# Optimization experiments

Measured on AMD Instinct MI355X. Metric: run time of the kernel, lower is better.

The kernel has to match this reference:

```python
import jax, jax.numpy as jnp
import numpy as np

ISO = 0.0
# cube corner k has coords ((k>>0)&1, (k>>1)&1, (k>>2)&1)
CORNERS = np.array([[(k >> 0) & 1, (k >> 1) & 1, (k >> 2) & 1] for k in range(8)], np.int32)
# 6-tetrahedra decomposition of the cube around body diagonal 0-7
TETS = np.array([[0,1,3,7],[0,3,2,7],[0,2,6,7],[0,6,4,7],[0,4,5,7],[0,5,1,7]], np.int32)
TET_EDGES = np.array([[0,1],[0,2],[0,3],[1,2],[1,3],[2,3]], np.int32)
# marching-tetrahedra triangle table: sign case -> up to 2 triangles of tet-edge ids (-1 = pad)
MT_TRI = np.array([
 [-1,-1,-1,-1,-1,-1],
 [0,1,2,-1,-1,-1],
 [0,3,4,-1,-1,-1],
 [1,2,4,1,4,3],
 [1,3,5,-1,-1,-1],
 [0,2,5,0,5,3],
 [0,1,5,0,5,4],
 [2,4,5,-1,-1,-1],
 [2,4,5,-1,-1,-1],
 [0,1,5,0,5,4],
 [0,3,5,0,5,2],
 [1,3,5,-1,-1,-1],
 [1,3,4,1,4,2],
 [0,3,4,-1,-1,-1],
 [0,1,2,-1,-1,-1],
 [-1,-1,-1,-1,-1,-1]], np.int32)

# map (tet, tet-edge) -> unique per-cell edge slot; enumerate unique corner pairs
_pairs, _edges = {}, []
T2C = np.zeros((6, 6), np.int32)
for _ti in range(6):
    for _ei in range(6):
        _a = int(TETS[_ti, TET_EDGES[_ei, 0]]); _b = int(TETS[_ti, TET_EDGES[_ei, 1]])
        _key = (min(_a, _b), max(_a, _b))
        if _key not in _pairs:
            _pairs[_key] = len(_edges); _edges.append(_key)
        T2C[_ti, _ei] = _pairs[_key]
CELL_EDGES = np.array(_edges, np.int32)  # (19, 2)
N_EDGE = len(_edges)


def _forward(sdfsgrid, featgrid, isovalue=ISO):
    X, Y, Z = sdfsgrid.shape
    F = featgrid.shape[-1]
    dt = sdfsgrid.dtype
    # pad like the torch wrapper: sdf border = isovalue+1 (outside), features = 0
    s = jnp.pad(sdfsgrid, 1, constant_values=isovalue + 1.0)
    f = jnp.pad(featgrid, ((1, 1), (1, 1), (1, 1), (0, 0)))
    cx, cy, cz = s.shape[0] - 1, s.shape[1] - 1, s.shape[2] - 1
    # per-cell corner values: (cx,cy,cz,8) and (cx,cy,cz,8,F)
    cs = jnp.stack([s[dx:dx + cx, dy:dy + cy, dz:dz + cz] for dx, dy, dz in CORNERS], axis=-1)
    cf = jnp.stack([f[dx:dx + cx, dy:dy + cy, dz:dz + cz] for dx, dy, dz in CORNERS], axis=-2)
    inside = cs < isovalue
    ea, eb = CELL_EDGES[:, 0], CELL_EDGES[:, 1]
    sa, sb = cs[..., ea], cs[..., eb]                      # (cx,cy,cz,19)
    cross = inside[..., ea] != inside[..., eb]
    t = jnp.where(cross, (isovalue - sa) / jnp.where(cross, sb - sa, 1.0), 0.0)
    base = jnp.stack(jnp.meshgrid(jnp.arange(cx), jnp.arange(cy), jnp.arange(cz), indexing='ij'), axis=-1).astype(dt)
    pa = base[..., None, :] + jnp.asarray(CORNERS[ea], dt)  # (.,19,3)
    pb = base[..., None, :] + jnp.asarray(CORNERS[eb], dt)
    verts = pa + t[..., None] * (pb - pa)
    fa = jnp.take(cf, ea, axis=3)
    fb = jnp.take(cf, eb, axis=3)
    feats = fa + t[..., None] * (fb - fa)                  # (.,19,F)
    verts = jnp.where(cross[..., None], verts, 0.0)
    feats = jnp.where(cross[..., None], feats, 0.0)
    # triangles: per-tet sign case, table lookup, remap to per-cell edge slots
    bits = inside[..., TETS].astype(jnp.int32)             # (.,6,4)
    case = bits[..., 0] + 2 * bits[..., 1] + 4 * bits[..., 2] + 8 * bits[..., 3]
    ltri = jnp.asarray(MT_TRI)[case]                       # (.,6,6)
    ce = jnp.asarray(T2C)[jnp.arange(6)[:, None], jnp.clip(ltri, 0)]
    cell_lin = jnp.arange(cx * cy * cz, dtype=jnp.int32).reshape(cx, cy, cz)
    gid = jnp.where(ltri >= 0, cell_lin[..., None, None] * N_EDGE + ce, -1)
    tris = gid.reshape(-1, 3).astype(jnp.int32)
    scale = jnp.asarray([X, Y, Z], dt) - 1.0
    verts = (verts.reshape(-1, 3) - 1.0) / scale           # undo pad offset, normalize
    feats = feats.reshape(-1, F)
    return verts, feats, tris


def setup_inputs() -> dict:
    key = jax.random.key(0)
    k1, k2 = jax.random.split(key)
    sdfsgrid = jax.random.normal(k1, (64, 64, 64), jnp.float32)
    featgrid = jax.random.normal(k2, (64, 64, 64, 8), jnp.float32)
    return {"sdfsgrid": sdfsgrid, "featgrid": featgrid}


def reference(sdfsgrid, featgrid):
    return _forward(sdfsgrid, featgrid)
```

## Files before the change

### kernel.cpp

```cpp
#include <hip/hip_runtime.h>

#define NC 65
#define NCELL 274625
#define NE 19
#define NF 8

__constant__ unsigned MTP[16] = {
    0x00FFFFFFu, 0x00FFF210u, 0x00FFF430u, 0x00341421u,
    0x00FFF531u, 0x00350520u, 0x00450510u, 0x00FFF542u,
    0x00FFF542u, 0x00450510u, 0x00250530u, 0x00FFF531u,
    0x00241431u, 0x00FFF430u, 0x00FFF210u, 0x00FFFFFFu
};

__constant__ unsigned T2CPc[6] = {
    0x0A418820u, 0x105388C1u, 0x16850926u,
    0x1CB68989u, 0x22E809ECu, 0x0919080Fu
};

__device__ constexpr int EA[NE] = {0,0,0,1,1,3,0,2,2,0,2,6,0,4,4,0,4,5,1};
__device__ constexpr int EB[NE] = {1,3,7,3,7,7,2,3,7,6,6,7,4,6,7,5,5,7,5};
#define EAP 0x006C120C82419200ULL
#define EBP 0x017DBF4FB76BF7D9ULL
#define TETP 0x36C9B24D9ULL

typedef float float4u __attribute__((ext_vector_type(4), aligned(4)));
typedef float float2u __attribute__((ext_vector_type(2), aligned(4)));

extern "C" __global__ void __launch_bounds__(256, 4)
diffmc_kernel(const float* __restrict__ sdf, const float* __restrict__ feat,
              float* __restrict__ oV, float* __restrict__ oF, float* __restrict__ oT)
{
    __shared__ float lds[256 * 21];
    const int tid = threadIdx.x;
    const int blockBase = blockIdx.x << 8;
    int vc = NCELL - blockBase;
    vc = vc > 256 ? 256 : vc;

    if (tid < vc) {
        const int cell = blockBase + tid;
        const int k  = cell % NC;
        const int t_ = cell / NC;
        const int j  = t_ % NC;
        const int i  = t_ / NC;
        float cs[8];
#pragma unroll
        for (int c = 0; c < 8; ++c) {
            int x = i + (c & 1) - 1;
            int y = j + ((c >> 1) & 1) - 1;
            int z = k + ((c >> 2) & 1) - 1;
            bool inb = ((unsigned)x < 64u) & ((unsigned)y < 64u) & ((unsigned)z < 64u);
            cs[c] = inb ? sdf[(x * 64 + y) * 64 + z] : 1.0f;
        }
        unsigned ins = 0;
#pragma unroll
        for (int c = 0; c < 8; ++c) ins |= (cs[c] < 0.0f ? 1u : 0u) << c;
        float* Ld = lds + tid * 21;
#pragma unroll
        for (int e = 0; e < NE; ++e) {
            const int a = EA[e], b = EB[e];
            bool cross = ((ins >> a) ^ (ins >> b)) & 1u;
            Ld[e] = cross ? (-cs[a]) / (cs[b] - cs[a]) : 0.0f;
        }
        Ld[19] = __uint_as_float(ins);
        Ld[20] = __uint_as_float((unsigned)i | ((unsigned)j << 7) | ((unsigned)k << 14));
    }
    __syncthreads();

    const float inv63 = 1.0f / 63.0f;

    {
        const int nE = vc * NE;
        float* __restrict__ dV = oV + (size_t)blockBase * 57;
        float* __restrict__ dF = oF + (size_t)blockBase * 152;
        for (int E = tid; E < nE; E += 256) {
            const unsigned c = (unsigned)E / 19u;
            const unsigned e = (unsigned)E - c * 19u;
            const float    t    = lds[c * 21 + e];
            const unsigned meta = __float_as_uint(lds[c * 21 + 20]);
            const unsigned ii = meta & 127u;
            const unsigned jj = (meta >> 7) & 127u;
            const unsigned kk = (meta >> 14) & 127u;
            const unsigned a = (unsigned)(EAP >> (3u * e)) & 7u;
            const unsigned b = (unsigned)(EBP >> (3u * e)) & 7u;
            const bool cross = t > 0.0f;

            const float pax = (float)(int)(ii + (a & 1u));
            const float pbx = (float)(int)(ii + (b & 1u));
            const float pay = (float)(int)(jj + ((a >> 1) & 1u));
            const float pby = (float)(int)(jj + ((b >> 1) & 1u));
            const float paz = (float)(int)(kk + ((a >> 2) & 1u));
            const float pbz = (float)(int)(kk + ((b >> 2) & 1u));
            const float vx = cross ? pax + t * (pbx - pax) : 0.0f;
            const float vy = cross ? pay + t * (pby - pay) : 0.0f;
            const float vz = cross ? paz + t * (pbz - paz) : 0.0f;
            const size_t vo = (size_t)c * 57 + e * 3u;
            dV[vo + 0] = (vx - 1.0f) * inv63;
            dV[vo + 1] = (vy - 1.0f) * inv63;
            dV[vo + 2] = (vz - 1.0f) * inv63;

            const int xa = (int)ii + (int)(a & 1u) - 1;
            const int ya = (int)jj + (int)((a >> 1) & 1u) - 1;
            const int za = (int)kk + (int)((a >> 2) & 1u) - 1;
            const int xb = (int)ii + (int)(b & 1u) - 1;
            const int yb = (int)jj + (int)((b >> 1) & 1u) - 1;
            const int zb = (int)kk + (int)((b >> 2) & 1u) - 1;
            const bool iba = ((unsigned)xa < 64u) & ((unsigned)ya < 64u) & ((unsigned)za < 64u);
            const bool ibb = ((unsigned)xb < 64u) & ((unsigned)yb < 64u) & ((unsigned)zb < 64u);
            float4 fa0 = make_float4(0.f, 0.f, 0.f, 0.f), fa1 = fa0;
            float4 fb0 = fa0, fb1 = fa0;
            if (iba) {
                const float4* fp = (const float4*)(feat + (size_t)((xa * 64 + ya) * 64 + za) * NF);
                fa0 = fp[0]; fa1 = fp[1];
            }
            if (ibb) {
                const float4* fp = (const float4*)(feat + (size_t)((xb * 64 + yb) * 64 + zb) * NF);
                fb0 = fp[0]; fb1 = fp[1];
            }
            float4u flo, fhi;
            flo.x = cross ? fa0.x + t * (fb0.x - fa0.x) : 0.0f;
            flo.y = cross ? fa0.y + t * (fb0.y - fa0.y) : 0.0f;
            flo.z = cross ? fa0.z + t * (fb0.z - fa0.z) : 0.0f;
            flo.w = cross ? fa0.w + t * (fb0.w - fa0.w) : 0.0f;
            fhi.x = cross ? fa1.x + t * (fb1.x - fa1.x) : 0.0f;
            fhi.y = cross ? fa1.y + t * (fb1.y - fa1.y) : 0.0f;
            fhi.z = cross ? fa1.z + t * (fb1.z - fa1.z) : 0.0f;
            fhi.w = cross ? fa1.w + t * (fb1.w - fa1.w) : 0.0f;
            const size_t fo = (size_t)c * 152 + e * 8u;
            *(float4u*)(dF + fo)     = flo;
            *(float4u*)(dF + fo + 4) = fhi;
        }
    }

    {
        const int nT = vc * 6;
        float* __restrict__ dT = oT + (size_t)blockBase * 36;
        for (int T = tid; T < nT; T += 256) {
            const unsigned c  = (unsigned)T / 6u;
            const unsigned ti = (unsigned)T - c * 6u;
            const unsigned ins = __float_as_uint(lds[c * 21 + 19]);
            const unsigned tc = (unsigned)(TETP >> (6u * ti)) & 63u;
            const unsigned c1 = tc & 7u, c2 = tc >> 3;
            const unsigned cse = (ins & 1u)
                               | (((ins >> c1) & 1u) << 1)
                               | (((ins >> c2) & 1u) << 2)
                               | (((ins >> 7) & 1u) << 3);
            const unsigned m  = MTP[cse];
            const unsigned tp = T2CPc[ti];
            const int cell19 = (blockBase + (int)c) * 19;
            float v6[6];
#pragma unroll
            for (int v = 0; v < 6; ++v) {
                const unsigned lt = (m >> (4 * v)) & 0xFu;
                const unsigned lc = (lt == 15u) ? 0u : lt;
                const unsigned ce = (tp >> (5 * lc)) & 31u;
                v6[v] = (lt == 15u) ? -1.0f : (float)(cell19 + (int)ce);
            }
            const size_t to = (size_t)c * 36 + ti * 6u;
            float4u q0; q0.x = v6[0]; q0.y = v6[1]; q0.z = v6[2]; q0.w = v6[3];
            float2u q1; q1.x = v6[4]; q1.y = v6[5];
            *(float4u*)(dT + to)     = q0;
            *(float2u*)(dT + to + 4) = q1;
        }
    }
}

extern "C" void kernel_launch(void* const* d_in, const int* in_sizes, int n_in,
                              void* d_out, int out_size, void* d_ws, size_t ws_size,
                              hipStream_t stream) {
    const float* sdf  = (const float*)d_in[0];
    const float* feat = (const float*)d_in[1];
    float* out = (float*)d_out;
    float* oV = out;
    float* oF = oV + (size_t)NCELL * NE * 3;
    float* oT = oF + (size_t)NCELL * NE * NF;
    int blocks = (NCELL + 255) / 256;
    diffmc_kernel<<<blocks, 256, 0, stream>>>(sdf, feat, oV, oF, oT);
}
```

Before: 57.53 us.

## Store corner SDFs in LDS, compute edge t lazily, swizzle blocks across XCDs

Phase one now writes the 8 corner SDF values, the inside mask and the packed coordinates to LDS (stride 11) instead of precomputing all 19 edge interpolation parameters (stride 21). The second phase reads the two corner values per edge and computes the crossing test and t itself. This shrinks LDS use and removes per-thread divides from phase one. Block indices are remapped so consecutive cell ranges land on the same XCD for L2 locality, and the loops become fixed-count with unroll 2. The trade-off is that the per-edge division moves into the store loop, and the changed crossing test may round differently from the previous t computation.

Result: no change. 57.81 us (+0.5%).

```diff
diff --git a/kernel.cpp b/kernel.cpp
--- a/kernel.cpp
+++ b/kernel.cpp
@@ -26,13 +26,21 @@
 typedef float float4u __attribute__((ext_vector_type(4), aligned(4)));
 typedef float float2u __attribute__((ext_vector_type(2), aligned(4)));
 
+#define LSTR 11
+
 extern "C" __global__ void __launch_bounds__(256, 4)
 diffmc_kernel(const float* __restrict__ sdf, const float* __restrict__ feat,
               float* __restrict__ oV, float* __restrict__ oF, float* __restrict__ oT)
 {
-    __shared__ float lds[256 * 21];
+    __shared__ float lds[256 * LSTR];
     const int tid = threadIdx.x;
-    const int blockBase = blockIdx.x << 8;
+
+    const int nwg = gridDim.x;
+    const int q = nwg >> 3, r = nwg & 7;
+    const int xcd = blockIdx.x & 7, s = blockIdx.x >> 3;
+    const int swz = xcd * q + (xcd < r ? xcd : r) + s;
+
+    const int blockBase = swz << 8;
     int vc = NCELL - blockBase;
     vc = vc > 256 ? 256 : vc;
 
@@ -54,35 +62,37 @@
         unsigned ins = 0;
 #pragma unroll
         for (int c = 0; c < 8; ++c) ins |= (cs[c] < 0.0f ? 1u : 0u) << c;
-        float* Ld = lds + tid * 21;
+        float* Ld = lds + tid * LSTR;
 #pragma unroll
-        for (int e = 0; e < NE; ++e) {
-            const int a = EA[e], b = EB[e];
-            bool cross = ((ins >> a) ^ (ins >> b)) & 1u;
-            Ld[e] = cross ? (-cs[a]) / (cs[b] - cs[a]) : 0.0f;
-        }
-        Ld[19] = __uint_as_float(ins);
-        Ld[20] = __uint_as_float((unsigned)i | ((unsigned)j << 7) | ((unsigned)k << 14));
+        for (int c = 0; c < 8; ++c) Ld[c] = cs[c];
+        Ld[8] = __uint_as_float(ins);
+        Ld[9] = __uint_as_float((unsigned)i | ((unsigned)j << 7) | ((unsigned)k << 14));
     }
     __syncthreads();
 
     const float inv63 = 1.0f / 63.0f;
+    const int nE = vc * NE;
+    const int nT = vc * 6;
 
     {
-        const int nE = vc * NE;
         float* __restrict__ dV = oV + (size_t)blockBase * 57;
         float* __restrict__ dF = oF + (size_t)blockBase * 152;
-        for (int E = tid; E < nE; E += 256) {
+#pragma unroll 2
+        for (int rr = 0; rr < 19; ++rr) {
+            const int E = tid + (rr << 8);
+            if (E >= nE) break;
             const unsigned c = (unsigned)E / 19u;
             const unsigned e = (unsigned)E - c * 19u;
-            const float    t    = lds[c * 21 + e];
-            const unsigned meta = __float_as_uint(lds[c * 21 + 20]);
+            const float* Ld = lds + c * LSTR;
+            const unsigned meta = __float_as_uint(Ld[9]);
             const unsigned ii = meta & 127u;
             const unsigned jj = (meta >> 7) & 127u;
             const unsigned kk = (meta >> 14) & 127u;
             const unsigned a = (unsigned)(EAP >> (3u * e)) & 7u;
             const unsigned b = (unsigned)(EBP >> (3u * e)) & 7u;
-            const bool cross = t > 0.0f;
+            const float sa = Ld[a], sb = Ld[b];
+            const bool cross = (sa < 0.0f) != (sb < 0.0f);
+            const float t = cross ? sa / (sa - sb) : 0.0f;
 
             const float pax = (float)(int)(ii + (a & 1u));
             const float pbx = (float)(int)(ii + (b & 1u));
@@ -93,7 +103,7 @@
             const float vx = cross ? pax + t * (pbx - pax) : 0.0f;
             const float vy = cross ? pay + t * (pby - pay) : 0.0f;
             const float vz = cross ? paz + t * (pbz - paz) : 0.0f;
-            const size_t vo = (size_t)c * 57 + e * 3u;
+            const size_t vo = (size_t)E * 3u;
             dV[vo + 0] = (vx - 1.0f) * inv63;
             dV[vo + 1] = (vy - 1.0f) * inv63;
             dV[vo + 2] = (vz - 1.0f) * inv63;
@@ -125,19 +135,21 @@
             fhi.y = cross ? fa1.y + t * (fb1.y - fa1.y) : 0.0f;
             fhi.z = cross ? fa1.z + t * (fb1.z - fa1.z) : 0.0f;
             fhi.w = cross ? fa1.w + t * (fb1.w - fa1.w) : 0.0f;
-            const size_t fo = (size_t)c * 152 + e * 8u;
+            const size_t fo = (size_t)E * 8u;
             *(float4u*)(dF + fo)     = flo;
             *(float4u*)(dF + fo + 4) = fhi;
         }
     }
 
     {
-        const int nT = vc * 6;
         float* __restrict__ dT = oT + (size_t)blockBase * 36;
-        for (int T = tid; T < nT; T += 256) {
+#pragma unroll 2
+        for (int rr = 0; rr < 6; ++rr) {
+            const int T = tid + (rr << 8);
+            if (T >= nT) break;
             const unsigned c  = (unsigned)T / 6u;
             const unsigned ti = (unsigned)T - c * 6u;
-            const unsigned ins = __float_as_uint(lds[c * 21 + 19]);
+            const unsigned ins = __float_as_uint(lds[c * LSTR + 8]);
             const unsigned tc = (unsigned)(TETP >> (6u * ti)) & 63u;
             const unsigned c1 = tc & 7u, c2 = tc >> 3;
             const unsigned cse = (ins & 1u)
@@ -155,7 +167,7 @@
                 const unsigned ce = (tp >> (5 * lc)) & 31u;
                 v6[v] = (lt == 15u) ? -1.0f : (float)(cell19 + (int)ce);
             }
-            const size_t to = (size_t)c * 36 + ti * 6u;
+            const size_t to = (size_t)T * 6u;
             float4u q0; q0.x = v6[0]; q0.y = v6[1]; q0.z = v6[2]; q0.w = v6[3];
             float2u q1; q1.x = v6[4]; q1.y = v6[5];
             *(float4u*)(dT + to)     = q0;
```
